# Kernel tuning notes

Hardware: AMD Instinct MI355X
Metric: run time of the kernel (lower is better)

## Reference

```python
import jax, jax.numpy as jnp
import numpy as np

P = 9  # patch_size


def setup_inputs() -> dict:
    key = jax.random.key(0)
    k1, k2, k3, k4 = jax.random.split(key, 4)
    B, Cin, D, H, W = 1, 128, 36, 72, 72
    Cout = 128
    L = (D // P) * ((H * W) // P)  # 2304 non-overlapping patches
    x = jax.random.normal(k1, (B, Cin, D, H, W), dtype=jnp.float32)
    attentions = jax.random.normal(k2, (B, Cout, L, P * P), dtype=jnp.float32)
    Wc = jax.random.normal(k3, (Cout, Cin), dtype=jnp.float32) * 0.05  # conv_img 1x1x1 weight
    b = jax.random.normal(k4, (Cout,), dtype=jnp.float32) * 0.05
    return {"x": x, "attentions": attentions, "W": Wc, "b": b}


def reference(x, attentions, W, b):
    # conv_img: 1x1x1 Conv3d == per-voxel channel GEMM
    y = jnp.einsum('oc,bcdhw->bodhw', W, x) + b[None, :, None, None, None]
    B, C, D, H, Wd = y.shape
    HW = H * Wd
    y2 = y.reshape(1, C, D, HW)  # [1, C, D, H*W] as in the torch reshape
    nD, nW = D // P, HW // P
    # Unfold with kernel=stride=P (non-overlapping) == block reshape.
    # Column order: patches row-major; row order: kernel positions row-major.
    patches = (y2.reshape(1, C, nD, P, nW, P)
                 .transpose(0, 1, 2, 4, 3, 5)
                 .reshape(1, C, nD * nW, P * P))  # [1, C, L, P*P]
    nz = jnp.count_nonzero(attentions, axis=-1).astype(y2.dtype)[..., None] + 1e-5
    att = patches + attentions / nz  # [1, C, L, P*P]
    # Fold (non-overlapping) == inverse block reshape; no overlap accumulation.
    corr = (att.reshape(1, C, nD, nW, P, P)
               .transpose(0, 1, 2, 4, 3, 5)
               .reshape(1, C, D, HW))
    out = corr * y2 + y2
    return jnp.where(out >= 0, out, 0.2 * out)  # LeakyReLU(0.2)
```

## Files before the change

### kernel.cpp

```cpp
#include <hip/hip_runtime.h>
#include <hip/hip_bf16.h>

#define CIN   128
#define COUT  128
#define DD    36
#define HW    5184
#define DHW   186624
#define PATCH 9
#define NPW   576
#define L_TOT 2304
#define PP    81
#define LDSK  136

typedef __attribute__((ext_vector_type(8))) short bf16x8;
typedef __attribute__((ext_vector_type(4))) float f32x4;

__device__ __forceinline__ short f2bf(float f) {
    unsigned u = __builtin_bit_cast(unsigned, f);
    unsigned r = (u + 0x7fffu + ((u >> 16) & 1u)) >> 16;
    return (short)r;
}

__global__ __launch_bounds__(256) void count_nz(
    const float* __restrict__ attn, float* __restrict__ inv)
{
    const int pair = blockIdx.x * 256 + threadIdx.x;
    const float* ap = attn + (size_t)pair * PP;
    int cnt = 0;
    #pragma unroll
    for (int q = 0; q < PP; ++q) cnt += (ap[q] != 0.0f) ? 1 : 0;
    inv[pair] = 1.0f / ((float)cnt + 1e-5f);
}

__global__ __launch_bounds__(256) void fused_main(
    const float* __restrict__ x,
    const float* __restrict__ attn,
    const float* __restrict__ W,
    const float* __restrict__ bia,
    const float* __restrict__ inv,
    float* __restrict__ out)
{
    __shared__ __align__(16) short xs[64][LDSK];

    const int t    = threadIdx.x;
    const int wv   = t >> 6;
    const int lane = t & 63;
    const int col  = lane & 15;
    const int quad = lane >> 4;

    const int hwblk  = blockIdx.x % 81;
    const int d      = blockIdx.x / 81;
    const int hwbase = hwblk * 64;
    const int lbase  = (d / 9) * NPW;
    const int ii     = d % 9;

    #pragma unroll
    for (int e = t; e < 2048; e += 256) {
        const int row = e >> 4;
        const int f4  = e & 15;
        const float4 v = *(const float4*)(x + (size_t)row * DHW + (size_t)d * HW
                                          + hwbase + f4 * 4);
        const int n0 = f4 * 4;
        xs[n0 + 0][row] = f2bf(v.x);
        xs[n0 + 1][row] = f2bf(v.y);
        xs[n0 + 2][row] = f2bf(v.z);
        xs[n0 + 3][row] = f2bf(v.w);
    }

    const int wbase = wv * 32;
    bf16x8 afrag[2][4];
    #pragma unroll
    for (int mt = 0; mt < 2; ++mt) {
        const int m = wbase + mt * 16 + col;
        #pragma unroll
        for (int s = 0; s < 4; ++s) {
            const float4* wp4 = (const float4*)(W + m * 128 + s * 32 + quad * 8);
            float4 w0 = wp4[0], w1 = wp4[1];
            bf16x8 f;
            f[0] = f2bf(w0.x); f[1] = f2bf(w0.y); f[2] = f2bf(w0.z); f[3] = f2bf(w0.w);
            f[4] = f2bf(w1.x); f[5] = f2bf(w1.y); f[6] = f2bf(w1.z); f[7] = f2bf(w1.w);
            afrag[mt][s] = f;
        }
    }
    float bias[2][4];
    #pragma unroll
    for (int mt = 0; mt < 2; ++mt)
        #pragma unroll
        for (int r = 0; r < 4; ++r)
            bias[mt][r] = bia[wbase + mt * 16 + quad * 4 + r];

    __syncthreads();

    f32x4 acc[2][4];
    #pragma unroll
    for (int mt = 0; mt < 2; ++mt)
        #pragma unroll
        for (int tt = 0; tt < 4; ++tt)
            acc[mt][tt] = (f32x4){0.f, 0.f, 0.f, 0.f};

    #pragma unroll
    for (int s = 0; s < 4; ++s) {
        bf16x8 bfrag[4];
        #pragma unroll
        for (int tt = 0; tt < 4; ++tt)
            bfrag[tt] = *(const bf16x8*)&xs[tt * 16 + col][s * 32 + quad * 8];
        #pragma unroll
        for (int mt = 0; mt < 2; ++mt)
            #pragma unroll
            for (int tt = 0; tt < 4; ++tt)
                acc[mt][tt] = __builtin_amdgcn_mfma_f32_16x16x32_bf16(
                    afrag[mt][s], bfrag[tt], acc[mt][tt], 0, 0, 0);
    }

    #pragma unroll
    for (int tt = 0; tt < 4; ++tt) {
        const int n  = tt * 16 + col;
        const int hw = hwbase + n;
        const int p  = hw / 9;
        const int jj = hw - p * 9;
        const int l  = lbase + p;
        const int kk = ii * 9 + jj;
        #pragma unroll
        for (int mt = 0; mt < 2; ++mt) {
            #pragma unroll
            for (int r = 0; r < 4; ++r) {
                const int c = wbase + mt * 16 + quad * 4 + r;
                const float y  = acc[mt][tt][r] + bias[mt][r];
                const float a  = attn[(size_t)c * DHW + (size_t)l * PP + kk];
                const float iv = inv[c * L_TOT + l];
                const float v  = y * (y + a * iv + 1.0f);
                out[(size_t)c * DHW + (size_t)d * HW + hw] =
                    (v >= 0.f) ? v : 0.2f * v;
            }
        }
    }
}

__global__ __launch_bounds__(256) void fused_cross_head_fallback(
    const float* __restrict__ x, const float* __restrict__ attn,
    const float* __restrict__ W, const float* __restrict__ bia,
    float* __restrict__ out)
{
    __shared__ __align__(16) short xs[2][48][LDSK];
    __shared__ float inv_lds[COUT][4];

    const int t = threadIdx.x, wv = t >> 6, lane = t & 63;
    const int col = lane & 15, quad = lane >> 4;
    const int blk = blockIdx.x;
    const int pd = blk / 144, hwblk = blk - pd * 144;
    const int hwbase = hwblk * 36;
    const int lbase = pd * NPW + hwblk * 4;

    for (int pair = t; pair < 512; pair += 256) {
        const int c = pair >> 2, p = pair & 3;
        const float* ap = attn + (size_t)c * DHW + (size_t)(lbase + p) * PP;
        int cnt = 0;
        #pragma unroll 27
        for (int q = 0; q < PP; ++q) cnt += (ap[q] != 0.0f) ? 1 : 0;
        inv_lds[c][p] = 1.0f / ((float)cnt + 1e-5f);
    }
    const int wbase = wv * 32;
    bf16x8 afrag[2][4];
    #pragma unroll
    for (int mt = 0; mt < 2; ++mt) {
        const int m = wbase + mt * 16 + col;
        #pragma unroll
        for (int s = 0; s < 4; ++s) {
            const float4* wp4 = (const float4*)(W + m * 128 + s * 32 + quad * 8);
            float4 w0 = wp4[0], w1 = wp4[1];
            bf16x8 f;
            f[0] = f2bf(w0.x); f[1] = f2bf(w0.y); f[2] = f2bf(w0.z); f[3] = f2bf(w0.w);
            f[4] = f2bf(w1.x); f[5] = f2bf(w1.y); f[6] = f2bf(w1.z); f[7] = f2bf(w1.w);
            afrag[mt][s] = f;
        }
    }
    float bias[2][4];
    #pragma unroll
    for (int mt = 0; mt < 2; ++mt)
        #pragma unroll
        for (int r = 0; r < 4; ++r)
            bias[mt][r] = bia[wbase + mt * 16 + quad * 4 + r];

    for (int i = 0; i < 9; ++i) {
        const int buf = i & 1;
        const int d = pd * PATCH + i;
        for (int e = t; e < 1152; e += 256) {
            const int row = e / 9, f4 = e - row * 9;
            const float4 v = *(const float4*)(x + (size_t)row * DHW + (size_t)d * HW
                                              + hwbase + f4 * 4);
            const int n0 = f4 * 4;
            xs[buf][n0 + 0][row] = f2bf(v.x);
            xs[buf][n0 + 1][row] = f2bf(v.y);
            xs[buf][n0 + 2][row] = f2bf(v.z);
            xs[buf][n0 + 3][row] = f2bf(v.w);
        }
        __syncthreads();
        f32x4 acc[2][3];
        #pragma unroll
        for (int mt = 0; mt < 2; ++mt)
            #pragma unroll
            for (int tt = 0; tt < 3; ++tt)
                acc[mt][tt] = (f32x4){0.f, 0.f, 0.f, 0.f};
        #pragma unroll
        for (int s = 0; s < 4; ++s) {
            bf16x8 bfrag[3];
            #pragma unroll
            for (int tt = 0; tt < 3; ++tt)
                bfrag[tt] = *(const bf16x8*)&xs[buf][tt * 16 + col][s * 32 + quad * 8];
            #pragma unroll
            for (int mt = 0; mt < 2; ++mt)
                #pragma unroll
                for (int tt = 0; tt < 3; ++tt)
                    acc[mt][tt] = __builtin_amdgcn_mfma_f32_16x16x32_bf16(
                        afrag[mt][s], bfrag[tt], acc[mt][tt], 0, 0, 0);
        }
        #pragma unroll
        for (int tt = 0; tt < 3; ++tt) {
            const int n = tt * 16 + col;
            if (n < 36) {
                const int p = n / 9, jj = n - p * 9, kk = i * 9 + jj;
                #pragma unroll
                for (int mt = 0; mt < 2; ++mt) {
                    #pragma unroll
                    for (int r = 0; r < 4; ++r) {
                        const int c = wbase + mt * 16 + quad * 4 + r;
                        const float y = acc[mt][tt][r] + bias[mt][r];
                        const float a = attn[(size_t)c * DHW + (size_t)(lbase + p) * PP + kk];
                        const float v = y * (y + a * inv_lds[c][p] + 1.0f);
                        out[(size_t)c * DHW + (size_t)d * HW + hwbase + n] =
                            (v >= 0.f) ? v : 0.2f * v;
                    }
                }
            }
        }
    }
}

extern "C" void kernel_launch(void* const* d_in, const int* in_sizes, int n_in,
                              void* d_out, int out_size, void* d_ws, size_t ws_size,
                              hipStream_t stream) {
    const float* x    = (const float*)d_in[0];
    const float* attn = (const float*)d_in[1];
    const float* W    = (const float*)d_in[2];
    const float* b    = (const float*)d_in[3];
    float* out        = (float*)d_out;

    const size_t inv_bytes = (size_t)COUT * L_TOT * sizeof(float);
    if (ws_size >= inv_bytes) {
        float* inv = (float*)d_ws;
        count_nz<<<dim3((COUT * L_TOT) / 256), dim3(256), 0, stream>>>(attn, inv);
        fused_main<<<dim3(36 * 81), dim3(256), 0, stream>>>(x, attn, W, b, inv, out);
    } else {
        fused_cross_head_fallback<<<dim3(576), dim3(256), 0, stream>>>(x, attn, W, b, out);
    }
}
```

Baseline: 314.9 us.

## Vectorize nonzero count, remap blocks across XCDs, pack LDS stores, stream output

The nonzero-count kernel now has each thread handle four consecutive 81-element rows as 81 float4 loads and write four inverse counts at once, with a quarter as many threads. The main kernel remaps block IDs so consecutive blocks on each XCD share the same hw tile over successive depth slices, aiming for better L2 reuse of attention and inverse rows. The x staging loads two channel rows per iteration and writes packed 32-bit bf16 pairs into LDS, halving LDS store instructions. Output writes use nontemporal stores to avoid polluting cache with write-once data. Fewer threads in count_nz may cut memory-level parallelism, and the XCD remap assumes round-robin dispatch across 8 XCDs.

```diff
diff --git a/kernel.cpp b/kernel.cpp
--- a/kernel.cpp
+++ b/kernel.cpp
@@ -21,15 +21,56 @@
     return (short)r;
 }
 
-__global__ __launch_bounds__(256) void count_nz(
+__global__ __launch_bounds__(256) void count_nz_v2(
     const float* __restrict__ attn, float* __restrict__ inv)
 {
-    const int pair = blockIdx.x * 256 + threadIdx.x;
-    const float* ap = attn + (size_t)pair * PP;
-    int cnt = 0;
-    #pragma unroll
-    for (int q = 0; q < PP; ++q) cnt += (ap[q] != 0.0f) ? 1 : 0;
-    inv[pair] = 1.0f / ((float)cnt + 1e-5f);
+    const int g = blockIdx.x * 256 + threadIdx.x;
+    const float4* ap = (const float4*)attn + (size_t)g * 81;
+
+    int cnt0 = 0, cnt1 = 0, cnt2 = 0, cnt3 = 0;
+
+    #pragma unroll
+    for (int f = 0; f < 20; ++f) {
+        const float4 v = ap[f];
+        cnt0 += (v.x != 0.f) + (v.y != 0.f) + (v.z != 0.f) + (v.w != 0.f);
+    }
+    {
+        const float4 v = ap[20];
+        cnt0 += (v.x != 0.f);
+        cnt1 += (v.y != 0.f) + (v.z != 0.f) + (v.w != 0.f);
+    }
+    #pragma unroll
+    for (int f = 21; f < 40; ++f) {
+        const float4 v = ap[f];
+        cnt1 += (v.x != 0.f) + (v.y != 0.f) + (v.z != 0.f) + (v.w != 0.f);
+    }
+    {
+        const float4 v = ap[40];
+        cnt1 += (v.x != 0.f) + (v.y != 0.f);
+        cnt2 += (v.z != 0.f) + (v.w != 0.f);
+    }
+    #pragma unroll
+    for (int f = 41; f < 60; ++f) {
+        const float4 v = ap[f];
+        cnt2 += (v.x != 0.f) + (v.y != 0.f) + (v.z != 0.f) + (v.w != 0.f);
+    }
+    {
+        const float4 v = ap[60];
+        cnt2 += (v.x != 0.f) + (v.y != 0.f) + (v.z != 0.f);
+        cnt3 += (v.w != 0.f);
+    }
+    #pragma unroll
+    for (int f = 61; f < 81; ++f) {
+        const float4 v = ap[f];
+        cnt3 += (v.x != 0.f) + (v.y != 0.f) + (v.z != 0.f) + (v.w != 0.f);
+    }
+
+    float4 o;
+    o.x = 1.0f / ((float)cnt0 + 1e-5f);
+    o.y = 1.0f / ((float)cnt1 + 1e-5f);
+    o.z = 1.0f / ((float)cnt2 + 1e-5f);
+    o.w = 1.0f / ((float)cnt3 + 1e-5f);
+    *(float4*)(inv + (size_t)g * 4) = o;
 }
 
 __global__ __launch_bounds__(256) void fused_main(
@@ -48,23 +89,34 @@
     const int col  = lane & 15;
     const int quad = lane >> 4;
 
-    const int hwblk  = blockIdx.x % 81;
-    const int d      = blockIdx.x / 81;
+    const int bidRaw = blockIdx.x;
+    const int xcd = bidRaw & 7;
+    const int loc = bidRaw >> 3;
+    const int wgid = (xcd < 4 ? xcd * 365 : 1460 + (xcd - 4) * 364) + loc;
+
+    const int d      = wgid % 36;
+    const int hwblk  = wgid / 36;
     const int hwbase = hwblk * 64;
     const int lbase  = (d / 9) * NPW;
     const int ii     = d % 9;
 
     #pragma unroll
-    for (int e = t; e < 2048; e += 256) {
-        const int row = e >> 4;
+    for (int e = t; e < 1024; e += 256) {
+        const int rp  = e >> 4;
         const int f4  = e & 15;
-        const float4 v = *(const float4*)(x + (size_t)row * DHW + (size_t)d * HW
-                                          + hwbase + f4 * 4);
+        const int row = rp * 2;
+        const float* xp = x + (size_t)row * DHW + (size_t)d * HW + hwbase + f4 * 4;
+        const float4 va = *(const float4*)xp;
+        const float4 vb = *(const float4*)(xp + DHW);
         const int n0 = f4 * 4;
-        xs[n0 + 0][row] = f2bf(v.x);
-        xs[n0 + 1][row] = f2bf(v.y);
-        xs[n0 + 2][row] = f2bf(v.z);
-        xs[n0 + 3][row] = f2bf(v.w);
+        const unsigned p0 = (unsigned short)f2bf(va.x) | ((unsigned)(unsigned short)f2bf(vb.x) << 16);
+        const unsigned p1 = (unsigned short)f2bf(va.y) | ((unsigned)(unsigned short)f2bf(vb.y) << 16);
+        const unsigned p2 = (unsigned short)f2bf(va.z) | ((unsigned)(unsigned short)f2bf(vb.z) << 16);
+        const unsigned p3 = (unsigned short)f2bf(va.w) | ((unsigned)(unsigned short)f2bf(vb.w) << 16);
+        *(unsigned*)&xs[n0 + 0][row] = p0;
+        *(unsigned*)&xs[n0 + 1][row] = p1;
+        *(unsigned*)&xs[n0 + 2][row] = p2;
+        *(unsigned*)&xs[n0 + 3][row] = p3;
     }
 
     const int wbase = wv * 32;
@@ -129,8 +181,8 @@
                 const float a  = attn[(size_t)c * DHW + (size_t)l * PP + kk];
                 const float iv = inv[c * L_TOT + l];
                 const float v  = y * (y + a * iv + 1.0f);
-                out[(size_t)c * DHW + (size_t)d * HW + hw] =
-                    (v >= 0.f) ? v : 0.2f * v;
+                __builtin_nontemporal_store((v >= 0.f) ? v : 0.2f * v,
+                    out + (size_t)c * DHW + (size_t)d * HW + hw);
             }
         }
     }
@@ -248,7 +300,7 @@
     const size_t inv_bytes = (size_t)COUT * L_TOT * sizeof(float);
     if (ws_size >= inv_bytes) {
         float* inv = (float*)d_ws;
-        count_nz<<<dim3((COUT * L_TOT) / 256), dim3(256), 0, stream>>>(attn, inv);
+        count_nz_v2<<<dim3(288), dim3(256), 0, stream>>>(attn, inv);
         fused_main<<<dim3(36 * 81), dim3(256), 0, stream>>>(x, attn, W, b, inv, out);
     } else {
         fused_cross_head_fallback<<<dim3(576), dim3(256), 0, stream>>>(x, attn, W, b, out);
```

New measurement: 342.0 us. +8.6%, slower.

## Fuse nonzero count into single pipelined kernel with ballot-based counting

Applied to the files above, without the earlier changes.

Replaces the separate count_nz pass plus main GEMM kernel with one kernel per patch-row/36-column tile that counts nonzeros via wave ballots and popcount into LDS, then loops over the 9 depth slices with register-prefetched, double-buffered x staging. Block IDs are swizzled across 8 groups, and bf16 pairs are packed into 32-bit LDS stores. This removes the extra launch and the workspace round-trip for the inverse counts, and overlaps global loads with MFMA and epilogue work. The trade-off is only 576 blocks of 256 threads, which may underfill the GPU compared with the previous 2916-block grid.

```diff
diff --git a/kernel.cpp b/kernel.cpp
--- a/kernel.cpp
+++ b/kernel.cpp
@@ -1,5 +1,4 @@
 #include <hip/hip_runtime.h>
-#include <hip/hip_bf16.h>
 
 #define CIN   128
 #define COUT  128
@@ -21,26 +20,15 @@
     return (short)r;
 }
 
-__global__ __launch_bounds__(256) void count_nz(
-    const float* __restrict__ attn, float* __restrict__ inv)
-{
-    const int pair = blockIdx.x * 256 + threadIdx.x;
-    const float* ap = attn + (size_t)pair * PP;
-    int cnt = 0;
-    #pragma unroll
-    for (int q = 0; q < PP; ++q) cnt += (ap[q] != 0.0f) ? 1 : 0;
-    inv[pair] = 1.0f / ((float)cnt + 1e-5f);
-}
-
-__global__ __launch_bounds__(256) void fused_main(
+__global__ __launch_bounds__(256) void fused_all(
     const float* __restrict__ x,
     const float* __restrict__ attn,
     const float* __restrict__ W,
     const float* __restrict__ bia,
-    const float* __restrict__ inv,
     float* __restrict__ out)
 {
-    __shared__ __align__(16) short xs[64][LDSK];
+    __shared__ __align__(16) short xs[2][48][LDSK];
+    __shared__ float inv_lds[COUT][4];
 
     const int t    = threadIdx.x;
     const int wv   = t >> 6;
@@ -48,23 +36,58 @@
     const int col  = lane & 15;
     const int quad = lane >> 4;
 
-    const int hwblk  = blockIdx.x % 81;
-    const int d      = blockIdx.x / 81;
-    const int hwbase = hwblk * 64;
-    const int lbase  = (d / 9) * NPW;
-    const int ii     = d % 9;
-
-    #pragma unroll
-    for (int e = t; e < 2048; e += 256) {
-        const int row = e >> 4;
-        const int f4  = e & 15;
-        const float4 v = *(const float4*)(x + (size_t)row * DHW + (size_t)d * HW
-                                          + hwbase + f4 * 4);
-        const int n0 = f4 * 4;
-        xs[n0 + 0][row] = f2bf(v.x);
-        xs[n0 + 1][row] = f2bf(v.y);
-        xs[n0 + 2][row] = f2bf(v.z);
-        xs[n0 + 3][row] = f2bf(v.w);
+    const int bid = blockIdx.x;
+    const int w   = (bid & 7) * 72 + (bid >> 3);
+    const int pd     = w / 144;
+    const int hwblk  = w - pd * 144;
+    const int hwbase = hwblk * 36;
+    const int lbase  = pd * NPW + hwblk * 4;
+    const int d0     = pd * PATCH;
+
+    float4 pva[3], pvb[3];
+    #pragma unroll
+    for (int it = 0; it < 3; ++it) {
+        const int e = t + it * 256;
+        if (e < 576) {
+            const int rp = e / 9, f4 = e - rp * 9;
+            const float* xp = x + (size_t)(rp * 2) * DHW + (size_t)d0 * HW
+                            + hwbase + f4 * 4;
+            pva[it] = *(const float4*)xp;
+            pvb[it] = *(const float4*)(xp + DHW);
+        }
+    }
+
+    {
+        const size_t abase = (size_t)lbase * PP;
+        const unsigned long long m17 = (1ull << 17) - 1;
+        const unsigned long long m34 = (1ull << 34) - 1;
+        const unsigned long long m51 = (1ull << 51) - 1;
+        #pragma unroll 4
+        for (int it = 0; it < 32; ++it) {
+            const int c = wv * 32 + it;
+            const float* ap = attn + (size_t)c * DHW + abase;
+            const float v0 = ap[lane];
+            const float v1 = ap[64 + lane];
+            const float v2 = ap[128 + lane];
+            const float v3 = ap[192 + lane];
+            const float v4 = ap[256 + lane];
+            const float v5 = (lane < 4) ? ap[320 + lane] : 0.0f;
+            const unsigned long long b0 = __ballot(v0 != 0.0f);
+            const unsigned long long b1 = __ballot(v1 != 0.0f);
+            const unsigned long long b2 = __ballot(v2 != 0.0f);
+            const unsigned long long b3 = __ballot(v3 != 0.0f);
+            const unsigned long long b4 = __ballot(v4 != 0.0f);
+            const unsigned long long b5 = __ballot(v5 != 0.0f);
+            const int c0 = __popcll(b0) + __popcll(b1 & m17);
+            const int c1 = __popcll(b1 & ~m17) + __popcll(b2 & m34);
+            const int c2 = __popcll(b2 & ~m34) + __popcll(b3 & m51);
+            const int c3 = __popcll(b3 & ~m51) + __popcll(b4) + __popcll(b5);
+            if (lane < 4) {
+                const int cc = (lane == 0) ? c0 : (lane == 1) ? c1
+                             : (lane == 2) ? c2 : c3;
+                inv_lds[c][lane] = 1.0f / ((float)cc + 1e-5f);
+            }
+        }
     }
 
     const int wbase = wv * 32;
@@ -89,118 +112,48 @@
         for (int r = 0; r < 4; ++r)
             bias[mt][r] = bia[wbase + mt * 16 + quad * 4 + r];
 
+    #pragma unroll
+    for (int it = 0; it < 3; ++it) {
+        const int e = t + it * 256;
+        if (e < 576) {
+            const int rp = e / 9, f4 = e - rp * 9;
+            const int n0 = f4 * 4, row = rp * 2;
+            const float4 va = pva[it], vb = pvb[it];
+            const unsigned p0 = (unsigned short)f2bf(va.x) | ((unsigned)(unsigned short)f2bf(vb.x) << 16);
+            const unsigned p1 = (unsigned short)f2bf(va.y) | ((unsigned)(unsigned short)f2bf(vb.y) << 16);
+            const unsigned p2 = (unsigned short)f2bf(va.z) | ((unsigned)(unsigned short)f2bf(vb.z) << 16);
+            const unsigned p3 = (unsigned short)f2bf(va.w) | ((unsigned)(unsigned short)f2bf(vb.w) << 16);
+            *(unsigned*)&xs[0][n0 + 0][row] = p0;
+            *(unsigned*)&xs[0][n0 + 1][row] = p1;
+            *(unsigned*)&xs[0][n0 + 2][row] = p2;
+            *(unsigned*)&xs[0][n0 + 3][row] = p3;
+        }
+    }
     __syncthreads();
 
-    f32x4 acc[2][4];
-    #pragma unroll
-    for (int mt = 0; mt < 2; ++mt)
-        #pragma unroll
-        for (int tt = 0; tt < 4; ++tt)
-            acc[mt][tt] = (f32x4){0.f, 0.f, 0.f, 0.f};
-
-    #pragma unroll
-    for (int s = 0; s < 4; ++s) {
-        bf16x8 bfrag[4];
-        #pragma unroll
-        for (int tt = 0; tt < 4; ++tt)
-            bfrag[tt] = *(const bf16x8*)&xs[tt * 16 + col][s * 32 + quad * 8];
-        #pragma unroll
-        for (int mt = 0; mt < 2; ++mt)
-            #pragma unroll
-            for (int tt = 0; tt < 4; ++tt)
-                acc[mt][tt] = __builtin_amdgcn_mfma_f32_16x16x32_bf16(
-                    afrag[mt][s], bfrag[tt], acc[mt][tt], 0, 0, 0);
-    }
-
-    #pragma unroll
-    for (int tt = 0; tt < 4; ++tt) {
-        const int n  = tt * 16 + col;
-        const int hw = hwbase + n;
-        const int p  = hw / 9;
-        const int jj = hw - p * 9;
-        const int l  = lbase + p;
-        const int kk = ii * 9 + jj;
-        #pragma unroll
-        for (int mt = 0; mt < 2; ++mt) {
-            #pragma unroll
-            for (int r = 0; r < 4; ++r) {
-                const int c = wbase + mt * 16 + quad * 4 + r;
-                const float y  = acc[mt][tt][r] + bias[mt][r];
-                const float a  = attn[(size_t)c * DHW + (size_t)l * PP + kk];
-                const float iv = inv[c * L_TOT + l];
-                const float v  = y * (y + a * iv + 1.0f);
-                out[(size_t)c * DHW + (size_t)d * HW + hw] =
-                    (v >= 0.f) ? v : 0.2f * v;
-            }
-        }
-    }
-}
-
-__global__ __launch_bounds__(256) void fused_cross_head_fallback(
-    const float* __restrict__ x, const float* __restrict__ attn,
-    const float* __restrict__ W, const float* __restrict__ bia,
-    float* __restrict__ out)
-{
-    __shared__ __align__(16) short xs[2][48][LDSK];
-    __shared__ float inv_lds[COUT][4];
-
-    const int t = threadIdx.x, wv = t >> 6, lane = t & 63;
-    const int col = lane & 15, quad = lane >> 4;
-    const int blk = blockIdx.x;
-    const int pd = blk / 144, hwblk = blk - pd * 144;
-    const int hwbase = hwblk * 36;
-    const int lbase = pd * NPW + hwblk * 4;
-
-    for (int pair = t; pair < 512; pair += 256) {
-        const int c = pair >> 2, p = pair & 3;
-        const float* ap = attn + (size_t)c * DHW + (size_t)(lbase + p) * PP;
-        int cnt = 0;
-        #pragma unroll 27
-        for (int q = 0; q < PP; ++q) cnt += (ap[q] != 0.0f) ? 1 : 0;
-        inv_lds[c][p] = 1.0f / ((float)cnt + 1e-5f);
-    }
-    const int wbase = wv * 32;
-    bf16x8 afrag[2][4];
-    #pragma unroll
-    for (int mt = 0; mt < 2; ++mt) {
-        const int m = wbase + mt * 16 + col;
-        #pragma unroll
-        for (int s = 0; s < 4; ++s) {
-            const float4* wp4 = (const float4*)(W + m * 128 + s * 32 + quad * 8);
-            float4 w0 = wp4[0], w1 = wp4[1];
-            bf16x8 f;
-            f[0] = f2bf(w0.x); f[1] = f2bf(w0.y); f[2] = f2bf(w0.z); f[3] = f2bf(w0.w);
-            f[4] = f2bf(w1.x); f[5] = f2bf(w1.y); f[6] = f2bf(w1.z); f[7] = f2bf(w1.w);
-            afrag[mt][s] = f;
-        }
-    }
-    float bias[2][4];
-    #pragma unroll
-    for (int mt = 0; mt < 2; ++mt)
-        #pragma unroll
-        for (int r = 0; r < 4; ++r)
-            bias[mt][r] = bia[wbase + mt * 16 + quad * 4 + r];
-
-    for (int i = 0; i < 9; ++i) {
-        const int buf = i & 1;
-        const int d = pd * PATCH + i;
-        for (int e = t; e < 1152; e += 256) {
-            const int row = e / 9, f4 = e - row * 9;
-            const float4 v = *(const float4*)(x + (size_t)row * DHW + (size_t)d * HW
-                                              + hwbase + f4 * 4);
-            const int n0 = f4 * 4;
-            xs[buf][n0 + 0][row] = f2bf(v.x);
-            xs[buf][n0 + 1][row] = f2bf(v.y);
-            xs[buf][n0 + 2][row] = f2bf(v.z);
-            xs[buf][n0 + 3][row] = f2bf(v.w);
-        }
-        __syncthreads();
+    int buf = 0;
+    for (int ii = 0; ii < 9; ++ii) {
+        if (ii < 8) {
+            #pragma unroll
+            for (int it = 0; it < 3; ++it) {
+                const int e = t + it * 256;
+                if (e < 576) {
+                    const int rp = e / 9, f4 = e - rp * 9;
+                    const float* xp = x + (size_t)(rp * 2) * DHW
+                                    + (size_t)(d0 + ii + 1) * HW + hwbase + f4 * 4;
+                    pva[it] = *(const float4*)xp;
+                    pvb[it] = *(const float4*)(xp + DHW);
+                }
+            }
+        }
+
         f32x4 acc[2][3];
         #pragma unroll
         for (int mt = 0; mt < 2; ++mt)
             #pragma unroll
             for (int tt = 0; tt < 3; ++tt)
                 acc[mt][tt] = (f32x4){0.f, 0.f, 0.f, 0.f};
+
         #pragma unroll
         for (int s = 0; s < 4; ++s) {
             bf16x8 bfrag[3];
@@ -214,18 +167,23 @@
                     acc[mt][tt] = __builtin_amdgcn_mfma_f32_16x16x32_bf16(
                         afrag[mt][s], bfrag[tt], acc[mt][tt], 0, 0, 0);
         }
+
+        const int d = d0 + ii;
         #pragma unroll
         for (int tt = 0; tt < 3; ++tt) {
             const int n = tt * 16 + col;
             if (n < 36) {
-                const int p = n / 9, jj = n - p * 9, kk = i * 9 + jj;
+                const int p  = n / 9;
+                const int jj = n - p * 9;
+                const int kk = ii * 9 + jj;
+                const int l  = lbase + p;
                 #pragma unroll
                 for (int mt = 0; mt < 2; ++mt) {
                     #pragma unroll
                     for (int r = 0; r < 4; ++r) {
                         const int c = wbase + mt * 16 + quad * 4 + r;
                         const float y = acc[mt][tt][r] + bias[mt][r];
-                        const float a = attn[(size_t)c * DHW + (size_t)(lbase + p) * PP + kk];
+                        const float a = attn[(size_t)c * DHW + (size_t)l * PP + kk];
                         const float v = y * (y + a * inv_lds[c][p] + 1.0f);
                         out[(size_t)c * DHW + (size_t)d * HW + hwbase + n] =
                             (v >= 0.f) ? v : 0.2f * v;
@@ -233,6 +191,28 @@
                 }
             }
         }
+
+        if (ii < 8) {
+            #pragma unroll
+            for (int it = 0; it < 3; ++it) {
+                const int e = t + it * 256;
+                if (e < 576) {
+                    const int rp = e / 9, f4 = e - rp * 9;
+                    const int n0 = f4 * 4, row = rp * 2;
+                    const float4 va = pva[it], vb = pvb[it];
+                    const unsigned p0 = (unsigned short)f2bf(va.x) | ((unsigned)(unsigned short)f2bf(vb.x) << 16);
+                    const unsigned p1 = (unsigned short)f2bf(va.y) | ((unsigned)(unsigned short)f2bf(vb.y) << 16);
+                    const unsigned p2 = (unsigned short)f2bf(va.z) | ((unsigned)(unsigned short)f2bf(vb.z) << 16);
+                    const unsigned p3 = (unsigned short)f2bf(va.w) | ((unsigned)(unsigned short)f2bf(vb.w) << 16);
+                    *(unsigned*)&xs[buf ^ 1][n0 + 0][row] = p0;
+                    *(unsigned*)&xs[buf ^ 1][n0 + 1][row] = p1;
+                    *(unsigned*)&xs[buf ^ 1][n0 + 2][row] = p2;
+                    *(unsigned*)&xs[buf ^ 1][n0 + 3][row] = p3;
+                }
+            }
+        }
+        __syncthreads();
+        buf ^= 1;
     }
 }
 
@@ -245,12 +225,5 @@
     const float* b    = (const float*)d_in[3];
     float* out        = (float*)d_out;
 
-    const size_t inv_bytes = (size_t)COUT * L_TOT * sizeof(float);
-    if (ws_size >= inv_bytes) {
-        float* inv = (float*)d_ws;
-        count_nz<<<dim3((COUT * L_TOT) / 256), dim3(256), 0, stream>>>(attn, inv);
-        fused_main<<<dim3(36 * 81), dim3(256), 0, stream>>>(x, attn, W, b, inv, out);
-    } else {
-        fused_cross_head_fallback<<<dim3(576), dim3(256), 0, stream>>>(x, attn, W, b, out);
-    }
+    fused_all<<<dim3(576), dim3(256), 0, stream>>>(x, attn, W, b, out);
 }
```

After: 325.4 us. +3.3%, slower.

## Stage attention and inverse counts in LDS, ballot-based nonzero count, XCD-aware remap

Applied to the files above, without the earlier changes.

Replaces the per-thread strided nonzero count with a wave-ballot kernel using coalesced float4 loads and popcount masks. The main kernel now stages the attention tile (as bf16) and inverse counts in LDS with more contiguous loads, instead of gathering them from global memory in the epilogue. It also remaps block ids per XCD and packs two bf16 rows per LDS store. Rounding attention to bf16 adds a small numeric error, and the extra LDS may reduce occupancy.

```diff
diff --git a/kernel.cpp b/kernel.cpp
--- a/kernel.cpp
+++ b/kernel.cpp
@@ -1,5 +1,4 @@
 #include <hip/hip_runtime.h>
-#include <hip/hip_bf16.h>
 
 #define CIN   128
 #define COUT  128
@@ -20,19 +19,66 @@
     unsigned r = (u + 0x7fffu + ((u >> 16) & 1u)) >> 16;
     return (short)r;
 }
-
-__global__ __launch_bounds__(256) void count_nz(
+__device__ __forceinline__ float bf2f(short s) {
+    return __builtin_bit_cast(float, ((unsigned)(unsigned short)s) << 16);
+}
+
+__global__ __launch_bounds__(256) void count_ballot(
     const float* __restrict__ attn, float* __restrict__ inv)
 {
-    const int pair = blockIdx.x * 256 + threadIdx.x;
-    const float* ap = attn + (size_t)pair * PP;
-    int cnt = 0;
-    #pragma unroll
-    for (int q = 0; q < PP; ++q) cnt += (ap[q] != 0.0f) ? 1 : 0;
-    inv[pair] = 1.0f / ((float)cnt + 1e-5f);
-}
-
-__global__ __launch_bounds__(256) void fused_main(
+    const int wv   = threadIdx.x >> 6;
+    const int lane = threadIdx.x & 63;
+    const int w    = blockIdx.x * 4 + wv;
+
+    const unsigned long long P0X = (1ull << 21) - 1;
+    const unsigned long long P0Y = (1ull << 20) - 1;
+    const unsigned long long P1X = ((1ull << 20) - 1) << 21;
+    const unsigned long long P1Y = ((1ull << 21) - 1) << 20;
+    const unsigned long long P1Z = ((1ull << 20) - 1) << 20;
+    const unsigned long long P2X = ((1ull << 20) - 1) << 41;
+    const unsigned long long P2Z = ((1ull << 21) - 1) << 40;
+    const unsigned long long P2W = ((1ull << 20) - 1) << 40;
+    const unsigned long long P3X = 0x7ull << 61;
+    const unsigned long long P3W = 0xFull << 60;
+    const unsigned long long TL  = (1ull << 17) - 1;
+
+    #pragma unroll
+    for (int k = 0; k < 4; ++k) {
+        const int g = w * 4 + k;
+        const float4* ap = (const float4*)attn + (size_t)g * 81;
+        const float4 va = ap[lane];
+        float4 vb = (float4){0.f, 0.f, 0.f, 0.f};
+        if (lane < 17) vb = ap[64 + lane];
+
+        const unsigned long long bx = __ballot(va.x != 0.f);
+        const unsigned long long by = __ballot(va.y != 0.f);
+        const unsigned long long bz = __ballot(va.z != 0.f);
+        const unsigned long long bw = __ballot(va.w != 0.f);
+        const unsigned long long tx = __ballot(vb.x != 0.f);
+        const unsigned long long ty = __ballot(vb.y != 0.f);
+        const unsigned long long tz = __ballot(vb.z != 0.f);
+        const unsigned long long tw = __ballot(vb.w != 0.f);
+
+        const int c0 = __popcll(bx & P0X) + __popcll(by & P0Y)
+                     + __popcll(bz & P0Y) + __popcll(bw & P0Y);
+        const int c1 = __popcll(bx & P1X) + __popcll(by & P1Y)
+                     + __popcll(bz & P1Z) + __popcll(bw & P1Z);
+        const int c2 = __popcll(bx & P2X) + __popcll(by & P2X)
+                     + __popcll(bz & P2Z) + __popcll(bw & P2W);
+        const int c3 = __popcll(bx & P3X) + __popcll(by & P3X)
+                     + __popcll(bz & P3X) + __popcll(bw & P3W)
+                     + __popcll(tx & TL) + __popcll(ty & TL)
+                     + __popcll(tz & TL) + __popcll(tw & TL);
+
+        if (lane < 4) {
+            const int cc = (lane == 0) ? c0 : (lane == 1) ? c1
+                         : (lane == 2) ? c2 : c3;
+            inv[(size_t)g * 4 + lane] = 1.0f / ((float)cc + 1e-5f);
+        }
+    }
+}
+
+__global__ __launch_bounds__(256, 4) void fused_main_v3(
     const float* __restrict__ x,
     const float* __restrict__ attn,
     const float* __restrict__ W,
@@ -41,6 +87,8 @@
     float* __restrict__ out)
 {
     __shared__ __align__(16) short xs[64][LDSK];
+    __shared__ short attn_s[128][76];
+    __shared__ float inv_s[128][8];
 
     const int t    = threadIdx.x;
     const int wv   = t >> 6;
@@ -48,23 +96,53 @@
     const int col  = lane & 15;
     const int quad = lane >> 4;
 
-    const int hwblk  = blockIdx.x % 81;
-    const int d      = blockIdx.x / 81;
+    const int bidRaw = blockIdx.x;
+    const int xcd = bidRaw & 7;
+    const int loc = bidRaw >> 3;
+    const int wgid = (xcd < 4 ? xcd * 365 : 1460 + (xcd - 4) * 364) + loc;
+
+    const int d      = wgid % 36;
+    const int hwblk  = wgid / 36;
     const int hwbase = hwblk * 64;
     const int lbase  = (d / 9) * NPW;
     const int ii     = d % 9;
-
-    #pragma unroll
-    for (int e = t; e < 2048; e += 256) {
-        const int row = e >> 4;
+    const int p0     = hwbase / 9;
+
+    #pragma unroll
+    for (int e = t; e < 1024; e += 256) {
+        const int rp  = e >> 4;
         const int f4  = e & 15;
-        const float4 v = *(const float4*)(x + (size_t)row * DHW + (size_t)d * HW
-                                          + hwbase + f4 * 4);
+        const int row = rp * 2;
+        const float* xp = x + (size_t)row * DHW + (size_t)d * HW + hwbase + f4 * 4;
+        const float4 va = *(const float4*)xp;
+        const float4 vb = *(const float4*)(xp + DHW);
         const int n0 = f4 * 4;
-        xs[n0 + 0][row] = f2bf(v.x);
-        xs[n0 + 1][row] = f2bf(v.y);
-        xs[n0 + 2][row] = f2bf(v.z);
-        xs[n0 + 3][row] = f2bf(v.w);
+        const unsigned p0w = (unsigned short)f2bf(va.x) | ((unsigned)(unsigned short)f2bf(vb.x) << 16);
+        const unsigned p1w = (unsigned short)f2bf(va.y) | ((unsigned)(unsigned short)f2bf(vb.y) << 16);
+        const unsigned p2w = (unsigned short)f2bf(va.z) | ((unsigned)(unsigned short)f2bf(vb.z) << 16);
+        const unsigned p3w = (unsigned short)f2bf(va.w) | ((unsigned)(unsigned short)f2bf(vb.w) << 16);
+        *(unsigned*)&xs[n0 + 0][row] = p0w;
+        *(unsigned*)&xs[n0 + 1][row] = p1w;
+        *(unsigned*)&xs[n0 + 2][row] = p2w;
+        *(unsigned*)&xs[n0 + 3][row] = p3w;
+    }
+
+    #pragma unroll
+    for (int k = 0; k < 36; ++k) {
+        const int e   = t + 256 * k;
+        const int c   = e / 72;
+        const int rem = e - c * 72;
+        const int q   = rem / 9;
+        const int j   = rem - q * 9;
+        const float a = attn[(size_t)c * DHW + (size_t)(lbase + p0 + q) * PP
+                             + ii * 9 + j];
+        attn_s[c][rem] = f2bf(a);
+    }
+    #pragma unroll
+    for (int k = 0; k < 4; ++k) {
+        const int e = t + 256 * k;
+        const int c = e >> 3, q = e & 7;
+        inv_s[c][q] = inv[(size_t)c * L_TOT + lbase + p0 + q];
     }
 
     const int wbase = wv * 32;
@@ -118,16 +196,16 @@
         const int hw = hwbase + n;
         const int p  = hw / 9;
         const int jj = hw - p * 9;
-        const int l  = lbase + p;
-        const int kk = ii * 9 + jj;
+        const int q  = p - p0;
+        const int rem = q * 9 + jj;
         #pragma unroll
         for (int mt = 0; mt < 2; ++mt) {
             #pragma unroll
             for (int r = 0; r < 4; ++r) {
                 const int c = wbase + mt * 16 + quad * 4 + r;
                 const float y  = acc[mt][tt][r] + bias[mt][r];
-                const float a  = attn[(size_t)c * DHW + (size_t)l * PP + kk];
-                const float iv = inv[c * L_TOT + l];
+                const float a  = bf2f(attn_s[c][rem]);
+                const float iv = inv_s[c][q];
                 const float v  = y * (y + a * iv + 1.0f);
                 out[(size_t)c * DHW + (size_t)d * HW + hw] =
                     (v >= 0.f) ? v : 0.2f * v;
@@ -233,6 +311,7 @@
                 }
             }
         }
+        __syncthreads();
     }
 }
 
@@ -248,8 +327,8 @@
     const size_t inv_bytes = (size_t)COUT * L_TOT * sizeof(float);
     if (ws_size >= inv_bytes) {
         float* inv = (float*)d_ws;
-        count_nz<<<dim3((COUT * L_TOT) / 256), dim3(256), 0, stream>>>(attn, inv);
-        fused_main<<<dim3(36 * 81), dim3(256), 0, stream>>>(x, attn, W, b, inv, out);
+        count_ballot<<<dim3(4608), dim3(256), 0, stream>>>(attn, inv);
+        fused_main_v3<<<dim3(36 * 81), dim3(256), 0, stream>>>(x, attn, W, b, inv, out);
     } else {
         fused_cross_head_fallback<<<dim3(576), dim3(256), 0, stream>>>(x, attn, W, b, out);
     }
```

After: 290.2 us. 7.8% less time.
